# Performance work log

Hardware: AMD Instinct MI355X
Metric: run time of the kernel (lower is better)

## Reference

```python
import jax, jax.numpy as jnp
import numpy as np

N = 50000   # num_nodes
T = 8       # num_time_steps
C = 64      # feature width (num_features == hidden == num_classes == 64, forced by the module's shape constraints)
E = 800000  # num_edges


def temporal_conv(x, edge_index, time_index, W, b, perturb=None):
    """Faithful TemporalAGNNConv.forward: per-timestep masked scatter-add of
    neighbor features, concat over T, linear + relu. Implemented as a single
    fused (t, dst)-bucketed segment reduce instead of T separate propagates.
    Note: self.lin is dead code in the original; self-loop addition in the
    original would crash (time_index length mismatch) so edges are used as-is.
    """
    src, dst = edge_index[0], edge_index[1]
    msgs = x[src]                                   # [E, C] gather
    seg = time_index * N + dst                      # combined (t, node) bucket
    agg = jax.ops.segment_sum(msgs, seg, num_segments=T * N)   # [T*N, C]
    cat = agg.reshape(T, N, C).transpose(1, 0, 2).reshape(N, T * C)  # [N, T*C]
    out = jax.nn.relu(cat @ W + b)                  # temporal_lin + relu
    if perturb is not None:
        out = out + perturb
    return out


def setup_inputs() -> dict:
    key = jax.random.key(0)
    ks = jax.random.split(key, 11)
    x = jax.random.normal(ks[0], (N, C), jnp.float32)
    edge_index = jax.random.randint(ks[1], (2, E), 0, N, dtype=jnp.int32)
    time_index = jax.random.randint(ks[2], (E,), 0, T, dtype=jnp.int32)
    s_t = 1.0 / np.sqrt(T * C).astype(np.float32)
    # temporal_lin weights stored as [in, out] (torch Linear transposed)
    Wt1 = jax.random.uniform(ks[3], (T * C, C), jnp.float32, -s_t, s_t)
    bt1 = jax.random.uniform(ks[4], (C,), jnp.float32, -s_t, s_t)
    Wt2 = jax.random.uniform(ks[5], (T * C, C), jnp.float32, -s_t, s_t)
    bt2 = jax.random.uniform(ks[6], (C,), jnp.float32, -s_t, s_t)
    s_a1 = 1.0 / np.sqrt(C).astype(np.float32)
    Wa1 = jax.random.uniform(ks[7], (C, 128), jnp.float32, -s_a1, s_a1)
    ba1 = jax.random.uniform(ks[8], (128,), jnp.float32, -s_a1, s_a1)
    s_a2 = 1.0 / np.sqrt(128).astype(np.float32)
    Wa2 = jax.random.uniform(ks[9], (128, C), jnp.float32, -s_a2, s_a2)
    ba2 = jax.random.uniform(ks[10], (C,), jnp.float32, -s_a2, s_a2)
    return {"x": x, "edge_index": edge_index, "time_index": time_index,
            "Wt1": Wt1, "bt1": bt1, "Wt2": Wt2, "bt2": bt2,
            "Wa1": Wa1, "ba1": ba1, "Wa2": Wa2, "ba2": ba2}


def reference(x, edge_index, time_index, Wt1, bt1, Wt2, bt2, Wa1, ba1, Wa2, ba2):
    h1 = jax.nn.relu(temporal_conv(x, edge_index, time_index, Wt1, bt1))   # conv1 + relu
    h2 = temporal_conv(h1, edge_index, time_index, Wt2, bt2)               # conv2 (output width C)
    adv = jax.nn.relu(h2 @ Wa1 + ba1) @ Wa2 + ba2                          # adversary MLP -> [N, C]
    out = temporal_conv(x, edge_index, time_index, Wt1, bt1, perturb=adv)  # conv1 again + perturbation
    return out
```

## Files before the change

### kernel.cpp

```cpp
#include <hip/hip_runtime.h>

#define N_NODES 50000
#define C_FEAT  64
#define E_EDGES 800000
#define KEYS    400000
#define NBLK1   391
#define DPB     16
#define NTILES  (N_NODES / DPB)
#define PBLK_X  1563
#define PBLK_W  128
#define PBLK_A  64
#define PBLK_H  391
#define DPART   6250

typedef __attribute__((ext_vector_type(8))) short short8;
typedef __attribute__((ext_vector_type(4))) float f32x4;

__device__ __forceinline__ float bf2f(unsigned short u) {
    union { unsigned int i; float f; } v; v.i = ((unsigned int)u) << 16; return v.f;
}
__device__ __forceinline__ unsigned short f2bf(float f) {
    union { float f; unsigned int i; } v; v.f = f;
    unsigned int r = v.i + 0x7fff + ((v.i >> 16) & 1);
    return (unsigned short)(r >> 16);
}

__global__ __launch_bounds__(256) void prep_hist(const float* __restrict__ x,
                                                 const float* __restrict__ W1,
                                                 const float* __restrict__ W2,
                                                 const float* __restrict__ Wa1,
                                                 const float* __restrict__ Wa2,
                                                 const int* __restrict__ dst,
                                                 const int* __restrict__ tix,
                                                 unsigned short* __restrict__ xb,
                                                 unsigned short* __restrict__ WT1,
                                                 unsigned short* __restrict__ WT2,
                                                 unsigned short* __restrict__ Wa1T,
                                                 unsigned short* __restrict__ Wa2T,
                                                 int* __restrict__ cnt) {
    const int b = blockIdx.x;
    if (b < PBLK_X) {
        int base = (b * 256 + threadIdx.x) * 8;
        if (base < N_NODES * 64) {
            float4 a = *(const float4*)(x + base);
            float4 c = *(const float4*)(x + base + 4);
            short8 o;
            o[0] = (short)f2bf(a.x); o[1] = (short)f2bf(a.y);
            o[2] = (short)f2bf(a.z); o[3] = (short)f2bf(a.w);
            o[4] = (short)f2bf(c.x); o[5] = (short)f2bf(c.y);
            o[6] = (short)f2bf(c.z); o[7] = (short)f2bf(c.w);
            *(short8*)(xb + base) = o;
        }
    } else if (b < PBLK_X + PBLK_W) {
        int i = (b - PBLK_X) * 256 + threadIdx.x;
        int n = i >> 9, k = i & 511;
        WT1[i] = f2bf(W1[k * 64 + n]);
        WT2[i] = f2bf(W2[k * 64 + n]);
    } else if (b < PBLK_X + PBLK_W + PBLK_A) {
        int i = (b - PBLK_X - PBLK_W) * 256 + threadIdx.x;
        if (i < 8192) {
            int n = i >> 6, k = i & 63;
            Wa1T[i] = f2bf(Wa1[k * 128 + n]);
        } else {
            int ii = i - 8192;
            int n = ii >> 7, k = ii & 127;
            Wa2T[ii] = f2bf(Wa2[k * 64 + n]);
        }
    } else {
        int bb = b - PBLK_X - PBLK_W - PBLK_A;
        const int e0 = bb * 2048 + threadIdx.x * 8;
        if (e0 < E_EDGES) {
            int4 d0 = *(const int4*)(dst + e0);
            int4 d1 = *(const int4*)(dst + e0 + 4);
            int4 t0 = *(const int4*)(tix + e0);
            int4 t1 = *(const int4*)(tix + e0 + 4);
            int dd[8] = {d0.x, d0.y, d0.z, d0.w, d1.x, d1.y, d1.z, d1.w};
            int tt[8] = {t0.x, t0.y, t0.z, t0.w, t1.x, t1.y, t1.z, t1.w};
            #pragma unroll
            for (int k = 0; k < 8; ++k)
                atomicAdd(&cnt[dd[k] * 8 + tt[k]], 1);
        }
    }
}

__global__ __launch_bounds__(256) void scan_all(int* __restrict__ cnt,
                                                int* __restrict__ bsum,
                                                int* __restrict__ chunkoff,
                                                int* __restrict__ done) {
    __shared__ int wsum[4];
    __shared__ int ticket;
    const int tid = threadIdx.x;
    const int lane = tid & 63;
    const int wave = tid >> 6;
    const int i4 = blockIdx.x * 256 + tid;
    int4 v = make_int4(0, 0, 0, 0);
    const bool ok = (i4 * 4 < KEYS);
    if (ok) v = ((const int4*)cnt)[i4];
    int s = v.x + v.y + v.z + v.w;
    int sc = s;
    #pragma unroll
    for (int d = 1; d < 64; d <<= 1) {
        int o = __shfl_up(sc, d, 64);
        if (lane >= d) sc += o;
    }
    if (lane == 63) wsum[wave] = sc;
    __syncthreads();
    int wbase = 0;
    #pragma unroll
    for (int w = 0; w < 4; ++w) wbase += (w < wave) ? wsum[w] : 0;
    int base = wbase + sc - s;
    int4 o;
    o.x = base;
    o.y = base + v.x;
    o.z = o.y + v.y;
    o.w = o.z + v.z;
    if (ok) ((int4*)cnt)[i4] = o;
    if (tid == 255) {
        bsum[blockIdx.x] = wbase + sc;
        __threadfence();
        ticket = atomicAdd(done, 1);
    }
    __syncthreads();
    if (ticket == NBLK1 - 1 && wave == 0) {
        int carry = 0;
        #pragma unroll
        for (int g = 0; g < (NBLK1 + 63) / 64; ++g) {
            int j = g * 64 + lane;
            int val = (j < NBLK1) ? atomicAdd(&bsum[j], 0) : 0;
            int scn = val;
            #pragma unroll
            for (int d = 1; d < 64; d <<= 1) {
                int oo = __shfl_up(scn, d, 64);
                if (lane >= d) scn += oo;
            }
            if (j < NBLK1) chunkoff[j] = carry + scn - val;
            carry += __shfl(scn, 63, 64);
        }
    }
}

__global__ __launch_bounds__(256) void scatter_edges(const int* __restrict__ src,
                                                     const int* __restrict__ dst,
                                                     const int* __restrict__ tix,
                                                     int* __restrict__ cursor,
                                                     const int* __restrict__ chunkoff,
                                                     int* __restrict__ elist) {
    const int g = blockIdx.x & 7;
    const int lo = g * DPART;
    const int e0 = (blockIdx.x >> 3) * 2048 + threadIdx.x * 8;
    if (e0 < E_EDGES) {
        int4 d0 = *(const int4*)(dst + e0);
        int4 d1 = *(const int4*)(dst + e0 + 4);
        int4 t0 = *(const int4*)(tix + e0);
        int4 t1 = *(const int4*)(tix + e0 + 4);
        int4 s0 = *(const int4*)(src + e0);
        int4 s1 = *(const int4*)(src + e0 + 4);
        int dd[8] = {d0.x, d0.y, d0.z, d0.w, d1.x, d1.y, d1.z, d1.w};
        int tt[8] = {t0.x, t0.y, t0.z, t0.w, t1.x, t1.y, t1.z, t1.w};
        int ss[8] = {s0.x, s0.y, s0.z, s0.w, s1.x, s1.y, s1.z, s1.w};
        #pragma unroll
        for (int k = 0; k < 8; ++k) {
            if ((unsigned)(dd[k] - lo) < (unsigned)DPART) {
                int key = dd[k] * 8 + tt[k];
                int pos = chunkoff[key >> 10] + atomicAdd(&cursor[key], 1);
                elist[pos] = ss[k] | (tt[k] << 16) | ((dd[k] & 15) << 19);
            }
        }
    }
}

#define FLUSH(P, V)                                                                   \
    { int _k = (P) >> 16;                                                             \
      if (_k != cur) { scat[cur >> 3][(cur & 7) * 64 + c] = f2bf(acc);                \
                       acc = 0.f; cur = _k; }                                         \
      acc += (V); }

#define EDGE(K)                                                                       \
    int p##K = __builtin_amdgcn_readlane(pv, e + K);                                  \
    float v##K = bf2f(Xb[(size_t)(p##K & 0xffff) * 64 + c]);

template <bool ADV>
__global__ __launch_bounds__(256, 8) void fused_conv(const unsigned short* __restrict__ Xb,
                                                     const unsigned short* __restrict__ WT,
                                                     const float* __restrict__ bias,
                                                     const int* __restrict__ segend,
                                                     const int* __restrict__ chunkoff,
                                                     const int* __restrict__ elist,
                                                     unsigned short* __restrict__ Hb,
                                                     const unsigned short* __restrict__ Wa1T,
                                                     const float* __restrict__ ba1,
                                                     const unsigned short* __restrict__ Wa2T,
                                                     const float* __restrict__ ba2,
                                                     const unsigned short* __restrict__ h1r,
                                                     float* __restrict__ outF) {
    __shared__ __attribute__((aligned(16))) unsigned short scat[DPB][520];
    unsigned short (*sH)[72]  = (unsigned short(*)[72])&scat[0][0];
    unsigned short (*sT)[136] = (unsigned short(*)[136])((char*)scat + 4096);
    const int lane = threadIdx.x & 63;
    const int wave = threadIdx.x >> 6;
    const int c = lane;
    const int dbase = blockIdx.x * DPB;

    {
        short8 z = {};
        *(short8*)&scat[wave * 4 + 0][lane * 8] = z;
        *(short8*)&scat[wave * 4 + 1][lane * 8] = z;
        *(short8*)&scat[wave * 4 + 2][lane * 8] = z;
        *(short8*)&scat[wave * 4 + 3][lane * 8] = z;
    }

    const int dquad = dbase + wave * 4;
    const int k0 = dquad * 8;
    const int sbeg = (dquad == 0) ? 0 : chunkoff[(k0 - 1) >> 10] + segend[k0 - 1];
    const int send = chunkoff[(k0 + 31) >> 10] + segend[k0 + 31];
    int pv = (lane < send - sbeg) ? elist[sbeg + lane] : 0;

    {
        int i = sbeg;
        int cur = 0;
        float acc = 0.f;
        if (i < send) cur = __builtin_amdgcn_readlane(pv, 0) >> 16;
        while (i < send) {
            int cnt = send - i; cnt = (cnt > 64) ? 64 : cnt;
            int pvn = 0;
            if (i + 64 < send) pvn = (lane < send - i - 64) ? elist[i + 64 + lane] : 0;
            int e = 0;
            for (; e + 15 < cnt; e += 16) {
                EDGE(0)  EDGE(1)  EDGE(2)  EDGE(3)
                EDGE(4)  EDGE(5)  EDGE(6)  EDGE(7)
                EDGE(8)  EDGE(9)  EDGE(10) EDGE(11)
                EDGE(12) EDGE(13) EDGE(14) EDGE(15)
                FLUSH(p0, v0)   FLUSH(p1, v1)   FLUSH(p2, v2)   FLUSH(p3, v3)
                FLUSH(p4, v4)   FLUSH(p5, v5)   FLUSH(p6, v6)   FLUSH(p7, v7)
                FLUSH(p8, v8)   FLUSH(p9, v9)   FLUSH(p10, v10) FLUSH(p11, v11)
                FLUSH(p12, v12) FLUSH(p13, v13) FLUSH(p14, v14) FLUSH(p15, v15)
            }
            if (e + 7 < cnt) {
                EDGE(0) EDGE(1) EDGE(2) EDGE(3) EDGE(4) EDGE(5) EDGE(6) EDGE(7)
                FLUSH(p0, v0) FLUSH(p1, v1) FLUSH(p2, v2) FLUSH(p3, v3)
                FLUSH(p4, v4) FLUSH(p5, v5) FLUSH(p6, v6) FLUSH(p7, v7)
                e += 8;
            }
            if (e + 3 < cnt) {
                EDGE(0) EDGE(1) EDGE(2) EDGE(3)
                FLUSH(p0, v0) FLUSH(p1, v1) FLUSH(p2, v2) FLUSH(p3, v3)
                e += 4;
            }
            if (e + 1 < cnt) {
                EDGE(0) EDGE(1)
                FLUSH(p0, v0) FLUSH(p1, v1)
                e += 2;
            }
            if (e < cnt) {
                EDGE(0)
                FLUSH(p0, v0)
            }
            i += 64;
            pv = pvn;
        }
        if (sbeg < send)
            scat[cur >> 3][(cur & 7) * 64 + c] = f2bf(acc);
    }
    __syncthreads();

    const int m = lane & 15;
    const int quad = lane >> 4;
    f32x4 acc4 = {0.f, 0.f, 0.f, 0.f};
    {
        const int n0 = wave * 16;
        const unsigned short* wrow = WT + (size_t)(n0 + m) * 512;
        #pragma unroll
        for (int kc = 0; kc < 16; ++kc) {
            short8 af = *(const short8*)&scat[m][kc * 32 + quad * 8];
            short8 bf = *(const short8*)(wrow + kc * 32 + quad * 8);
            acc4 = __builtin_amdgcn_mfma_f32_16x16x32_bf16(af, bf, acc4, 0, 0, 0);
        }
    }

    if (!ADV) {
        const int col = wave * 16 + m;
        const float bcol = bias[col];
        #pragma unroll
        for (int r = 0; r < 4; ++r) {
            int node = dbase + quad * 4 + r;
            Hb[(size_t)node * 64 + col] = f2bf(fmaxf(acc4[r] + bcol, 0.f));
        }
    } else {
        __syncthreads();
        {
            const int col = wave * 16 + m;
            const float bcol = bias[col];
            #pragma unroll
            for (int r = 0; r < 4; ++r)
                sH[quad * 4 + r][col] = f2bf(fmaxf(acc4[r] + bcol, 0.f));
        }
        __syncthreads();
        {
            #pragma unroll
            for (int ct = 0; ct < 2; ++ct) {
                f32x4 a1 = {0.f, 0.f, 0.f, 0.f};
                const int col = (wave * 2 + ct) * 16 + m;
                #pragma unroll
                for (int kc = 0; kc < 2; ++kc) {
                    short8 af = *(const short8*)&sH[m][kc * 32 + quad * 8];
                    short8 bf = *(const short8*)(Wa1T + (size_t)col * 64 + kc * 32 + quad * 8);
                    a1 = __builtin_amdgcn_mfma_f32_16x16x32_bf16(af, bf, a1, 0, 0, 0);
                }
                const float b1 = ba1[col];
                #pragma unroll
                for (int r = 0; r < 4; ++r)
                    sT[quad * 4 + r][col] = f2bf(fmaxf(a1[r] + b1, 0.f));
            }
        }
        __syncthreads();
        {
            f32x4 a2 = {0.f, 0.f, 0.f, 0.f};
            const int col = wave * 16 + m;
            #pragma unroll
            for (int kc = 0; kc < 4; ++kc) {
                short8 af = *(const short8*)&sT[m][kc * 32 + quad * 8];
                short8 bf = *(const short8*)(Wa2T + (size_t)col * 128 + kc * 32 + quad * 8);
                a2 = __builtin_amdgcn_mfma_f32_16x16x32_bf16(af, bf, a2, 0, 0, 0);
            }
            const float b2 = ba2[col];
            #pragma unroll
            for (int r = 0; r < 4; ++r) {
                int node = dbase + quad * 4 + r;
                outF[(size_t)node * 64 + col] =
                    a2[r] + b2 + bf2f(h1r[(size_t)node * 64 + col]);
            }
        }
    }
}

extern "C" void kernel_launch(void* const* d_in, const int* in_sizes, int n_in,
                              void* d_out, int out_size, void* d_ws, size_t ws_size,
                              hipStream_t stream) {
    const float* x   = (const float*)d_in[0];
    const int*   ei  = (const int*)d_in[1];
    const int*   tix = (const int*)d_in[2];
    const float* Wt1 = (const float*)d_in[3];
    const float* bt1 = (const float*)d_in[4];
    const float* Wt2 = (const float*)d_in[5];
    const float* bt2 = (const float*)d_in[6];
    const float* Wa1 = (const float*)d_in[7];
    const float* ba1 = (const float*)d_in[8];
    const float* Wa2 = (const float*)d_in[9];
    const float* ba2 = (const float*)d_in[10];
    float* out = (float*)d_out;

    const int* src = ei;
    const int* dst = ei + E_EDGES;

    unsigned short* xb   = (unsigned short*)d_ws;
    unsigned short* h1b  = xb + (size_t)N_NODES * 64;
    unsigned short* h2b  = h1b + (size_t)N_NODES * 64;
    unsigned short* WT1  = h2b + (size_t)N_NODES * 64;
    unsigned short* WT2  = WT1 + 64 * 512;
    unsigned short* Wa1T = WT2 + 64 * 512;
    unsigned short* Wa2T = Wa1T + 8192;
    int* cnt      = (int*)(Wa2T + 8192);
    int* bsum     = cnt + KEYS;
    int* chunkoff = bsum + 512;
    int* done     = chunkoff + 512;
    int* elist    = done + 64;

    hipMemsetAsync(cnt, 0, (KEYS + 512 + 512 + 64) * sizeof(int), stream);
    prep_hist<<<PBLK_X + PBLK_W + PBLK_A + PBLK_H, 256, 0, stream>>>(
        x, Wt1, Wt2, Wa1, Wa2, dst, tix, xb, WT1, WT2, Wa1T, Wa2T, cnt);
    scan_all<<<NBLK1, 256, 0, stream>>>(cnt, bsum, chunkoff, done);
    scatter_edges<<<8 * 391, 256, 0, stream>>>(src, dst, tix, cnt, chunkoff, elist);

    fused_conv<false><<<NTILES, 256, 0, stream>>>(
        xb, WT1, bt1, cnt, chunkoff, elist, h1b,
        nullptr, nullptr, nullptr, nullptr, nullptr, nullptr);
    fused_conv<true><<<NTILES, 256, 0, stream>>>(
        h1b, WT2, bt2, cnt, chunkoff, elist, nullptr,
        Wa1T, ba1, Wa2T, ba2, h1b, out);
}
```

Baseline: 271.4 us.

## Reuse histogram atomic ranks to scatter edges without a second atomic pass

```diff
diff --git a/kernel.cpp b/kernel.cpp
--- a/kernel.cpp
+++ b/kernel.cpp
@@ -11,7 +11,6 @@
 #define PBLK_W  128
 #define PBLK_A  64
 #define PBLK_H  391
-#define DPART   6250
 
 typedef __attribute__((ext_vector_type(8))) short short8;
 typedef __attribute__((ext_vector_type(4))) float f32x4;
@@ -30,6 +29,7 @@
                                                  const float* __restrict__ W2,
                                                  const float* __restrict__ Wa1,
                                                  const float* __restrict__ Wa2,
+                                                 const int* __restrict__ src,
                                                  const int* __restrict__ dst,
                                                  const int* __restrict__ tix,
                                                  unsigned short* __restrict__ xb,
@@ -37,7 +37,8 @@
                                                  unsigned short* __restrict__ WT2,
                                                  unsigned short* __restrict__ Wa1T,
                                                  unsigned short* __restrict__ Wa2T,
-                                                 int* __restrict__ cnt) {
+                                                 int* __restrict__ cnt,
+                                                 int2* __restrict__ rec) {
     const int b = blockIdx.x;
     if (b < PBLK_X) {
         int base = (b * 256 + threadIdx.x) * 8;
@@ -74,11 +75,19 @@
             int4 d1 = *(const int4*)(dst + e0 + 4);
             int4 t0 = *(const int4*)(tix + e0);
             int4 t1 = *(const int4*)(tix + e0 + 4);
+            int4 s0 = *(const int4*)(src + e0);
+            int4 s1 = *(const int4*)(src + e0 + 4);
             int dd[8] = {d0.x, d0.y, d0.z, d0.w, d1.x, d1.y, d1.z, d1.w};
             int tt[8] = {t0.x, t0.y, t0.z, t0.w, t1.x, t1.y, t1.z, t1.w};
+            int ss[8] = {s0.x, s0.y, s0.z, s0.w, s1.x, s1.y, s1.z, s1.w};
+            int rk[8];
             #pragma unroll
             for (int k = 0; k < 8; ++k)
-                atomicAdd(&cnt[dd[k] * 8 + tt[k]], 1);
+                rk[k] = atomicAdd(&cnt[dd[k] * 8 + tt[k]], 1);
+            #pragma unroll
+            for (int k = 0; k < 8; ++k)
+                rec[e0 + k] = make_int2(ss[k] | (tt[k] << 16) | ((dd[k] & 15) << 19),
+                                        (dd[k] * 8 + tt[k]) | (rk[k] << 19));
         }
     }
 }
@@ -139,33 +148,17 @@
     }
 }
 
-__global__ __launch_bounds__(256) void scatter_edges(const int* __restrict__ src,
-                                                     const int* __restrict__ dst,
-                                                     const int* __restrict__ tix,
-                                                     int* __restrict__ cursor,
-                                                     const int* __restrict__ chunkoff,
-                                                     int* __restrict__ elist) {
-    const int g = blockIdx.x & 7;
-    const int lo = g * DPART;
-    const int e0 = (blockIdx.x >> 3) * 2048 + threadIdx.x * 8;
-    if (e0 < E_EDGES) {
-        int4 d0 = *(const int4*)(dst + e0);
-        int4 d1 = *(const int4*)(dst + e0 + 4);
-        int4 t0 = *(const int4*)(tix + e0);
-        int4 t1 = *(const int4*)(tix + e0 + 4);
-        int4 s0 = *(const int4*)(src + e0);
-        int4 s1 = *(const int4*)(src + e0 + 4);
-        int dd[8] = {d0.x, d0.y, d0.z, d0.w, d1.x, d1.y, d1.z, d1.w};
-        int tt[8] = {t0.x, t0.y, t0.z, t0.w, t1.x, t1.y, t1.z, t1.w};
-        int ss[8] = {s0.x, s0.y, s0.z, s0.w, s1.x, s1.y, s1.z, s1.w};
-        #pragma unroll
-        for (int k = 0; k < 8; ++k) {
-            if ((unsigned)(dd[k] - lo) < (unsigned)DPART) {
-                int key = dd[k] * 8 + tt[k];
-                int pos = chunkoff[key >> 10] + atomicAdd(&cursor[key], 1);
-                elist[pos] = ss[k] | (tt[k] << 16) | ((dd[k] & 15) << 19);
-            }
-        }
+__global__ __launch_bounds__(256) void scatter_rank(const int2* __restrict__ rec,
+                                                    const int* __restrict__ cnt,
+                                                    const int* __restrict__ chunkoff,
+                                                    int* __restrict__ elist) {
+    const int i = (blockIdx.x * 256 + threadIdx.x) * 2;
+    if (i < E_EDGES) {
+        int4 r = *(const int4*)(rec + i);
+        int key0 = r.y & 0x7ffff, rank0 = (int)((unsigned)r.y >> 19);
+        int key1 = r.w & 0x7ffff, rank1 = (int)((unsigned)r.w >> 19);
+        elist[chunkoff[key0 >> 10] + cnt[key0] + rank0] = r.x;
+        elist[chunkoff[key1 >> 10] + cnt[key1] + rank1] = r.z;
     }
 }
 
@@ -183,7 +176,7 @@
 __global__ __launch_bounds__(256, 8) void fused_conv(const unsigned short* __restrict__ Xb,
                                                      const unsigned short* __restrict__ WT,
                                                      const float* __restrict__ bias,
-                                                     const int* __restrict__ segend,
+                                                     const int* __restrict__ cstart,
                                                      const int* __restrict__ chunkoff,
                                                      const int* __restrict__ elist,
                                                      unsigned short* __restrict__ Hb,
@@ -209,10 +202,10 @@
         *(short8*)&scat[wave * 4 + 3][lane * 8] = z;
     }
 
-    const int dquad = dbase + wave * 4;
-    const int k0 = dquad * 8;
-    const int sbeg = (dquad == 0) ? 0 : chunkoff[(k0 - 1) >> 10] + segend[k0 - 1];
-    const int send = chunkoff[(k0 + 31) >> 10] + segend[k0 + 31];
+    const int k0 = (dbase + wave * 4) * 8;
+    const int k1 = k0 + 32;
+    const int sbeg = chunkoff[k0 >> 10] + cstart[k0];
+    const int send = (k1 >= KEYS) ? E_EDGES : chunkoff[k1 >> 10] + cstart[k1];
     int pv = (lane < send - sbeg) ? elist[sbeg + lane] : 0;
 
     {
@@ -364,12 +357,13 @@
     int* chunkoff = bsum + 512;
     int* done     = chunkoff + 512;
     int* elist    = done + 64;
+    int2* rec     = (int2*)(elist + E_EDGES);
 
     hipMemsetAsync(cnt, 0, (KEYS + 512 + 512 + 64) * sizeof(int), stream);
     prep_hist<<<PBLK_X + PBLK_W + PBLK_A + PBLK_H, 256, 0, stream>>>(
-        x, Wt1, Wt2, Wa1, Wa2, dst, tix, xb, WT1, WT2, Wa1T, Wa2T, cnt);
+        x, Wt1, Wt2, Wa1, Wa2, src, dst, tix, xb, WT1, WT2, Wa1T, Wa2T, cnt, rec);
     scan_all<<<NBLK1, 256, 0, stream>>>(cnt, bsum, chunkoff, done);
-    scatter_edges<<<8 * 391, 256, 0, stream>>>(src, dst, tix, cnt, chunkoff, elist);
+    scatter_rank<<<(E_EDGES / 2 + 255) / 256, 256, 0, stream>>>(rec, cnt, chunkoff, elist);
 
     fused_conv<false><<<NTILES, 256, 0, stream>>>(
         xb, WT1, bt1, cnt, chunkoff, elist, h1b,
```

Result: faster. 253.6 us (-6.6%).
